# Kernel tuning notes

Hardware: AMD Instinct MI355X
Metric: run time of the kernel (lower is better)

## Reference

```python
import jax, jax.numpy as jnp
import numpy as np

EPS = 1e-5

def mish(x):
    return x * jnp.tanh(jax.nn.softplus(x))

def masked_bn(x, masks, w, b, rm, rv):
    # eval-mode masked batchnorm: normalize with running stats, zero masked-out positions
    out = w * ((x - rm) / jnp.sqrt(rv + EPS)) + b
    return jnp.where(masks, out, jnp.zeros((), dtype=out.dtype))

def channel_shuffle(x):
    B, C, L = x.shape
    cpg = C // 2
    y = jnp.pad(x, ((0, 0), (1, 1), (0, 0)))          # [B, C+2, L]
    y = y.reshape(B, 2, cpg + 1, L)
    y = jnp.transpose(y, (0, 2, 1, 3)).reshape(B, -1, L)
    return y[:, 1:-1, :]

def setup_inputs() -> dict:
    key = jax.random.key(0)
    ks = jax.random.split(key, 8)
    B, C, L = 32, 512, 4096
    br = C // 2
    x = jax.random.normal(ks[0], (B, C, L), dtype=jnp.float32)
    masks = jax.random.randint(ks[1], (B, 1, L), 0, 2) > 0
    s = 1.0 / np.sqrt(br)
    w1 = jax.random.normal(ks[2], (br, br, 1), dtype=jnp.float32) * s
    w2 = jax.random.normal(ks[3], (br, 1, 3), dtype=jnp.float32) * (1.0 / np.sqrt(3.0))
    w3 = jax.random.normal(ks[4], (br, br, 1), dtype=jnp.float32) * s
    def bn_params(k):
        k1, k2 = jax.random.split(k)
        return (jnp.ones((br, 1), jnp.float32), jnp.zeros((br, 1), jnp.float32),
                jax.random.normal(k1, (br, 1), jnp.float32) * 0.1,
                jnp.abs(jax.random.normal(k2, (br, 1), jnp.float32)) * 0.1 + 0.9)
    bn1 = bn_params(ks[5]); bn2 = bn_params(ks[6]); bn3 = bn_params(ks[7])
    return {"x": x, "masks": masks, "w1": w1, "w2": w2, "w3": w3,
            "bn1_w": bn1[0], "bn1_b": bn1[1], "bn1_rm": bn1[2], "bn1_rv": bn1[3],
            "bn2_w": bn2[0], "bn2_b": bn2[1], "bn2_rm": bn2[2], "bn2_rv": bn2[3],
            "bn3_w": bn3[0], "bn3_b": bn3[1], "bn3_rm": bn3[2], "bn3_rv": bn3[3]}

def reference(x, masks, w1, w2, w3,
              bn1_w, bn1_b, bn1_rm, bn1_rv,
              bn2_w, bn2_b, bn2_rm, bn2_rv,
              bn3_w, bn3_b, bn3_rm, bn3_rv):
    C = x.shape[1]
    x1, x2 = x[:, :C // 2, :], x[:, C // 2:, :]
    br = C // 2
    # conv_1: 1x1 pointwise -> GEMM
    b2 = jnp.einsum('oi,bil->bol', w1[:, :, 0], x2)
    b2 = mish(b2)
    b2 = masked_bn(b2, masks, bn1_w, bn1_b, bn1_rm, bn1_rv)
    # conv_2: depthwise k=3, pad=1
    b2 = jax.lax.conv_general_dilated(
        b2, w2, window_strides=(1,), padding=((1, 1),),
        dimension_numbers=('NCH', 'OIH', 'NCH'), feature_group_count=br)
    b2 = masked_bn(b2, masks, bn2_w, bn2_b, bn2_rm, bn2_rv)
    # conv_3: 1x1 pointwise
    b2 = jnp.einsum('oi,bil->bol', w3[:, :, 0], b2)
    b2 = mish(b2)
    b2 = masked_bn(b2, masks, bn3_w, bn3_b, bn3_rm, bn3_rv)
    # dropout: identity in eval mode
    out = jnp.concatenate([x1, b2], axis=1)
    return channel_shuffle(out)
```

## Files before the change

kernel.cpp:

```cpp
#include <hip/hip_runtime.h>
#include <cmath>

#define BATCH 32
#define CIN   512
#define BR    256
#define LEN   4096
#define TL    32
#define ROWS  34
#define RS    264
#define NBLK  128

typedef __attribute__((ext_vector_type(8))) short bf16x8;
typedef __attribute__((ext_vector_type(4))) float f32x4;

#define MFMA_BF16(a,b,c) __builtin_amdgcn_mfma_f32_16x16x32_bf16((a),(b),(c),0,0,0)

__device__ __forceinline__ float bf2f(unsigned short h){
  union { unsigned int u; float f; } c; c.u = ((unsigned int)h) << 16; return c.f;
}
__device__ __forceinline__ unsigned short f2bf(float f){
  union { float f; unsigned int u; } c; c.f = f;
  unsigned int r = c.u + 0x7fffu + ((c.u >> 16) & 1u);
  return (unsigned short)(r >> 16);
}
__device__ __forceinline__ float mish_f(float v){
  float p = __expf(fminf(v, 40.0f));
  float u = p * (p + 2.0f);
  return v * (u / (u + 2.0f));
}
__device__ __forceinline__ void unpack8(const uint4 v, float* f){
  f[0] = bf2f((unsigned short)(v.x & 0xffffu)); f[1] = bf2f((unsigned short)(v.x >> 16));
  f[2] = bf2f((unsigned short)(v.y & 0xffffu)); f[3] = bf2f((unsigned short)(v.y >> 16));
  f[4] = bf2f((unsigned short)(v.z & 0xffffu)); f[5] = bf2f((unsigned short)(v.z >> 16));
  f[6] = bf2f((unsigned short)(v.w & 0xffffu)); f[7] = bf2f((unsigned short)(v.w >> 16));
}

__global__ void prep_kernel(const float* __restrict__ w1, const float* __restrict__ w2,
                            const float* __restrict__ w3,
                            const float* __restrict__ b1w, const float* __restrict__ b1b,
                            const float* __restrict__ b1rm, const float* __restrict__ b1rv,
                            const float* __restrict__ b2w, const float* __restrict__ b2b,
                            const float* __restrict__ b2rm, const float* __restrict__ b2rv,
                            const float* __restrict__ b3w, const float* __restrict__ b3b,
                            const float* __restrict__ b3rm, const float* __restrict__ b3rv,
                            unsigned short* __restrict__ w1bf, unsigned short* __restrict__ w3bf,
                            float* __restrict__ folds)
{
  const int g = blockIdx.x * 256 + threadIdx.x;
  w1bf[g] = f2bf(w1[g]);
  w3bf[g] = f2bf(w3[g]);
  if (blockIdx.x == 0) {
    const int c = threadIdx.x;
    float a1 = b1w[c] / sqrtf(b1rv[c] + 1e-5f);
    folds[c]        = a1; folds[256 + c]  = b1b[c] - b1rm[c] * a1;
    float a2 = b2w[c] / sqrtf(b2rv[c] + 1e-5f);
    folds[512 + c]  = a2; folds[768 + c]  = b2b[c] - b2rm[c] * a2;
    float a3 = b3w[c] / sqrtf(b3rv[c] + 1e-5f);
    folds[1024 + c] = a3; folds[1280 + c] = b3b[c] - b3rm[c] * a3;
    folds[1536 + c] = w2[c * 3 + 0];
    folds[1792 + c] = w2[c * 3 + 1];
    folds[2048 + c] = w2[c * 3 + 2];
  }
}

__global__ __launch_bounds__(256, 4)
void fused_main(const float* __restrict__ xg,
                const int*   __restrict__ maskg,
                const unsigned short* __restrict__ w1bf,
                const unsigned short* __restrict__ w3bf,
                const float* __restrict__ fa1, const float* __restrict__ fb1,
                const float* __restrict__ fa2, const float* __restrict__ fb2,
                const float* __restrict__ fa3, const float* __restrict__ fb3,
                const float* __restrict__ w2p,
                float*       __restrict__ outg)
{
  __shared__ __align__(16) unsigned short ls_x2[ROWS * RS];
  __shared__ __align__(16) unsigned short ls_t1[ROWS * RS];

  const int tid = threadIdx.x;
  const int bx  = blockIdx.x;
  const int b   = blockIdx.y;
  const int l0  = bx * TL;

  {
    const size_t nchunks = (size_t)BATCH * BR * LEN / 4;
    const size_t stride  = (size_t)NBLK * BATCH * 256;
    for (size_t idx = ((size_t)b * NBLK + bx) * 256 + tid; idx < nchunks; idx += stride) {
      const int l  = (int)((idx & 1023) * 4);
      const int c  = (int)((idx >> 10) & 255);
      const int bb = (int)(idx >> 18);
      const float4 v = *(const float4*)(xg + (size_t)(bb * CIN + c) * LEN + l);
      *(float4*)(outg + (size_t)(bb * CIN + 2 * c + 1) * LEN + l) = v;
    }
  }

  if (bx == 0 || bx == NBLK - 1) {
    uint4* z = (uint4*)ls_x2;
    const uint4 zz = make_uint4(0, 0, 0, 0);
    for (int i = tid; i < (ROWS * RS) / 8; i += 256) z[i] = zz;
  }
  __syncthreads();

  {
    const int lbase4 = l0 - 4;
    for (int q = tid; q < 256 * 10; q += 256) {
      const int c   = q / 10;
      const int j   = q - c * 10;
      const int lg  = lbase4 + j * 4;
      const int lgc = min(max(lg, 0), LEN - 4);
      const float4 v = *(const float4*)(xg + (size_t)(b * CIN + BR + c) * LEN + lgc);
      const float vv[4] = {v.x, v.y, v.z, v.w};
      #pragma unroll
      for (int jj = 0; jj < 4; ++jj) {
        const int p = (lgc + jj) - (l0 - 1);
        if (p >= 0 && p < ROWS) ls_x2[p * RS + c] = f2bf(vv[jj]);
      }
    }
  }
  __syncthreads();

  const int lane = tid & 63;
  const int wid  = tid >> 6;
  const int xl   = lane & 15;
  const int qd   = lane >> 4;

  {
    int mk1[3];
    #pragma unroll
    for (int j = 0; j < 3; ++j) {
      const int p = 16 * j + xl;
      const int l = l0 - 1 + p;
      mk1[j] = (p < ROWS && l >= 0 && l < LEN) ? maskg[b * LEN + l] : 0;
    }
    #pragma unroll
    for (int mi = 0; mi < 4; ++mi) {
      const int ob = (wid * 4 + mi) * 16;
      bf16x8 af[8];
      #pragma unroll
      for (int k = 0; k < 8; ++k)
        af[k] = *(const bf16x8*)&w1bf[(size_t)(ob + xl) * 256 + k * 32 + qd * 8];
      const f32x4 av = *(const f32x4*)&fa1[ob + 4 * qd];
      const f32x4 bv = *(const f32x4*)&fb1[ob + 4 * qd];
      #pragma unroll
      for (int j = 0; j < 3; ++j) {
        const int p  = 16 * j + xl;
        const int rp = min(p, ROWS - 1);
        bf16x8 bfr[8];
        #pragma unroll
        for (int k = 0; k < 8; ++k)
          bfr[k] = *(const bf16x8*)&ls_x2[rp * RS + k * 32 + qd * 8];
        f32x4 acc = {0.f, 0.f, 0.f, 0.f};
        #pragma unroll
        for (int k = 0; k < 8; ++k) acc = MFMA_BF16(af[k], bfr[k], acc);
        unsigned short us[4];
        #pragma unroll
        for (int r = 0; r < 4; ++r) {
          float v = mish_f(acc[r]);
          v = av[r] * v + bv[r];
          if (!mk1[j]) v = 0.0f;
          us[r] = f2bf(v);
        }
        if (p < ROWS) {
          const unsigned int lo = (unsigned int)us[0] | ((unsigned int)us[1] << 16);
          const unsigned int hi = (unsigned int)us[2] | ((unsigned int)us[3] << 16);
          *(uint2*)&ls_t1[p * RS + ob + 4 * qd] = make_uint2(lo, hi);
        }
      }
    }
  }
  __syncthreads();

  {
    const int c0    = (tid & 31) * 8;
    const int qbase = tid >> 5;
    const f32x4 k0a = *(const f32x4*)&w2p[      c0], k0b = *(const f32x4*)&w2p[      c0 + 4];
    const f32x4 k1a = *(const f32x4*)&w2p[256 + c0], k1b = *(const f32x4*)&w2p[256 + c0 + 4];
    const f32x4 k2a = *(const f32x4*)&w2p[512 + c0], k2b = *(const f32x4*)&w2p[512 + c0 + 4];
    const f32x4 a2a = *(const f32x4*)&fa2[c0],       a2b = *(const f32x4*)&fa2[c0 + 4];
    const f32x4 b2a = *(const f32x4*)&fb2[c0],       b2b = *(const f32x4*)&fb2[c0 + 4];
    #pragma unroll
    for (int it = 0; it < 4; ++it) {
      const int qo = qbase + 8 * it;
      const int mk = maskg[b * LEN + l0 + qo];
      const uint4 ra = *(const uint4*)&ls_t1[(qo    ) * RS + c0];
      const uint4 rb = *(const uint4*)&ls_t1[(qo + 1) * RS + c0];
      const uint4 rc = *(const uint4*)&ls_t1[(qo + 2) * RS + c0];
      float ta[8], tb[8], tc[8];
      unpack8(ra, ta); unpack8(rb, tb); unpack8(rc, tc);
      unsigned short us[8];
      #pragma unroll
      for (int i = 0; i < 4; ++i) {
        float y  = a2a[i] * (k0a[i] * ta[i]     + k1a[i] * tb[i]     + k2a[i] * tc[i]    ) + b2a[i];
        float y2 = a2b[i] * (k0b[i] * ta[4 + i] + k1b[i] * tb[4 + i] + k2b[i] * tc[4 + i]) + b2b[i];
        if (!mk) { y = 0.0f; y2 = 0.0f; }
        us[i]     = f2bf(y);
        us[4 + i] = f2bf(y2);
      }
      uint4 wv;
      wv.x = (unsigned int)us[0] | ((unsigned int)us[1] << 16);
      wv.y = (unsigned int)us[2] | ((unsigned int)us[3] << 16);
      wv.z = (unsigned int)us[4] | ((unsigned int)us[5] << 16);
      wv.w = (unsigned int)us[6] | ((unsigned int)us[7] << 16);
      *(uint4*)&ls_x2[qo * RS + c0] = wv;
    }
  }
  __syncthreads();

  {
    int4 mku[2];
    #pragma unroll
    for (int j = 0; j < 2; ++j)
      mku[j] = *(const int4*)&maskg[b * LEN + l0 + 16 * j + 4 * qd];
    #pragma unroll
    for (int mi = 0; mi < 4; ++mi) {
      const int ob = (wid * 4 + mi) * 16;
      bf16x8 af[8];
      #pragma unroll
      for (int k = 0; k < 8; ++k)
        af[k] = *(const bf16x8*)&w3bf[(size_t)(ob + xl) * 256 + k * 32 + qd * 8];
      const float a3v = fa3[ob + xl];
      const float b3v = fb3[ob + xl];
      #pragma unroll
      for (int j = 0; j < 2; ++j) {
        bf16x8 ta2[8];
        #pragma unroll
        for (int k = 0; k < 8; ++k)
          ta2[k] = *(const bf16x8*)&ls_x2[(16 * j + xl) * RS + k * 32 + qd * 8];
        f32x4 acc = {0.f, 0.f, 0.f, 0.f};
        #pragma unroll
        for (int k = 0; k < 8; ++k) acc = MFMA_BF16(ta2[k], af[k], acc);
        const int4 mk = mku[j];
        const int mks[4] = {mk.x, mk.y, mk.z, mk.w};
        float4 ov;
        float* op = &ov.x;
        #pragma unroll
        for (int r = 0; r < 4; ++r) {
          float v = mish_f(acc[r]);
          v = a3v * v + b3v;
          if (!mks[r]) v = 0.0f;
          op[r] = v;
        }
        *(float4*)&outg[(size_t)(b * CIN + 2 * (ob + xl)) * LEN + l0 + 16 * j + 4 * qd] = ov;
      }
    }
  }
}

extern "C" void kernel_launch(void* const* d_in, const int* in_sizes, int n_in,
                              void* d_out, int out_size, void* d_ws, size_t ws_size,
                              hipStream_t stream) {
  (void)in_sizes; (void)n_in; (void)out_size; (void)ws_size;
  const float* xg    = (const float*)d_in[0];
  const int*   maskg = (const int*)d_in[1];
  const float* w1    = (const float*)d_in[2];
  const float* w2    = (const float*)d_in[3];
  const float* w3    = (const float*)d_in[4];
  const float* b1w   = (const float*)d_in[5];
  const float* b1b   = (const float*)d_in[6];
  const float* b1rm  = (const float*)d_in[7];
  const float* b1rv  = (const float*)d_in[8];
  const float* b2w   = (const float*)d_in[9];
  const float* b2b   = (const float*)d_in[10];
  const float* b2rm  = (const float*)d_in[11];
  const float* b2rv  = (const float*)d_in[12];
  const float* b3w   = (const float*)d_in[13];
  const float* b3b   = (const float*)d_in[14];
  const float* b3rm  = (const float*)d_in[15];
  const float* b3rv  = (const float*)d_in[16];
  float* outp = (float*)d_out;

  unsigned short* w1bf = (unsigned short*)d_ws;
  unsigned short* w3bf = (unsigned short*)((char*)d_ws + 131072);
  float*          folds = (float*)((char*)d_ws + 262144);

  hipLaunchKernelGGL(prep_kernel, dim3(256), dim3(256), 0, stream,
                     w1, w2, w3,
                     b1w, b1b, b1rm, b1rv, b2w, b2b, b2rm, b2rv, b3w, b3b, b3rm, b3rv,
                     w1bf, w3bf, folds);

  hipLaunchKernelGGL(fused_main, dim3(NBLK, BATCH, 1), dim3(256, 1, 1), 0, stream,
                     xg, maskg, w1bf, w3bf,
                     folds, folds + 256,
                     folds + 512, folds + 768,
                     folds + 1024, folds + 1280,
                     folds + 1536,
                     outp);
}
```

Baseline: 600.5 us.

## Split x1 passthrough copy into separate kernel, prefetch x2 tile, stage masks in LDS

Moves the x1 channel-interleave copy out of the fused kernel into a dedicated streaming copy kernel, so the fused kernel no longer runs a grid-stride copy loop. The x2 tile loads are issued up front into registers before the zero-fill and barrier, so they overlap with that work. Masks are loaded once per block into shared memory and reused by all three stages instead of being re-read from global memory. The cost is one extra kernel launch, and the fused kernel now holds ten float4 values in registers, which raises register pressure at its occupancy target of four blocks per SM.

```diff
diff --git a/kernel.cpp b/kernel.cpp
--- a/kernel.cpp
+++ b/kernel.cpp
@@ -63,6 +63,25 @@
   }
 }
 
+__global__ __launch_bounds__(256)
+void copy_x1_kernel(const float* __restrict__ xg, float* __restrict__ outg)
+{
+  const int k  = blockIdx.x;
+  const int bb = k >> 8;
+  const int c  = k & 255;
+  const float4* __restrict__ src = (const float4*)(xg  + (size_t)(bb * CIN + c)         * LEN);
+  float4*       __restrict__ dst = (float4*)      (outg + (size_t)(bb * CIN + 2 * c + 1) * LEN);
+  const int t = threadIdx.x;
+  const float4 v0 = src[t];
+  const float4 v1 = src[t + 256];
+  const float4 v2 = src[t + 512];
+  const float4 v3 = src[t + 768];
+  dst[t]       = v0;
+  dst[t + 256] = v1;
+  dst[t + 512] = v2;
+  dst[t + 768] = v3;
+}
+
 __global__ __launch_bounds__(256, 4)
 void fused_main(const float* __restrict__ xg,
                 const int*   __restrict__ maskg,
@@ -76,22 +95,22 @@
 {
   __shared__ __align__(16) unsigned short ls_x2[ROWS * RS];
   __shared__ __align__(16) unsigned short ls_t1[ROWS * RS];
+  __shared__ int ls_mk[48];
 
   const int tid = threadIdx.x;
   const int bx  = blockIdx.x;
   const int b   = blockIdx.y;
   const int l0  = bx * TL;
 
-  {
-    const size_t nchunks = (size_t)BATCH * BR * LEN / 4;
-    const size_t stride  = (size_t)NBLK * BATCH * 256;
-    for (size_t idx = ((size_t)b * NBLK + bx) * 256 + tid; idx < nchunks; idx += stride) {
-      const int l  = (int)((idx & 1023) * 4);
-      const int c  = (int)((idx >> 10) & 255);
-      const int bb = (int)(idx >> 18);
-      const float4 v = *(const float4*)(xg + (size_t)(bb * CIN + c) * LEN + l);
-      *(float4*)(outg + (size_t)(bb * CIN + 2 * c + 1) * LEN + l) = v;
-    }
+  float4 stg[10];
+  #pragma unroll
+  for (int it = 0; it < 10; ++it) {
+    const int q   = tid + 256 * it;
+    const int c   = q / 10;
+    const int j   = q - 10 * c;
+    const int lg  = l0 - 4 + 4 * j;
+    const int lgc = min(max(lg, 0), LEN - 4);
+    stg[it] = *(const float4*)(xg + (size_t)(b * CIN + BR + c) * LEN + lgc);
   }
 
   if (bx == 0 || bx == NBLK - 1) {
@@ -99,22 +118,24 @@
     const uint4 zz = make_uint4(0, 0, 0, 0);
     for (int i = tid; i < (ROWS * RS) / 8; i += 256) z[i] = zz;
   }
+  if (tid < 48) {
+    const int l = l0 - 1 + tid;
+    ls_mk[tid] = (tid < ROWS && l >= 0 && l < LEN) ? maskg[b * LEN + l] : 0;
+  }
   __syncthreads();
 
-  {
-    const int lbase4 = l0 - 4;
-    for (int q = tid; q < 256 * 10; q += 256) {
-      const int c   = q / 10;
-      const int j   = q - c * 10;
-      const int lg  = lbase4 + j * 4;
-      const int lgc = min(max(lg, 0), LEN - 4);
-      const float4 v = *(const float4*)(xg + (size_t)(b * CIN + BR + c) * LEN + lgc);
-      const float vv[4] = {v.x, v.y, v.z, v.w};
-      #pragma unroll
-      for (int jj = 0; jj < 4; ++jj) {
-        const int p = (lgc + jj) - (l0 - 1);
-        if (p >= 0 && p < ROWS) ls_x2[p * RS + c] = f2bf(vv[jj]);
-      }
+  #pragma unroll
+  for (int it = 0; it < 10; ++it) {
+    const int q   = tid + 256 * it;
+    const int c   = q / 10;
+    const int j   = q - 10 * c;
+    const int lg  = l0 - 4 + 4 * j;
+    const int lgc = min(max(lg, 0), LEN - 4);
+    const float vv[4] = {stg[it].x, stg[it].y, stg[it].z, stg[it].w};
+    #pragma unroll
+    for (int jj = 0; jj < 4; ++jj) {
+      const int p = (lgc + jj) - (l0 - 1);
+      if (p >= 0 && p < ROWS) ls_x2[p * RS + c] = f2bf(vv[jj]);
     }
   }
   __syncthreads();
@@ -127,11 +148,8 @@
   {
     int mk1[3];
     #pragma unroll
-    for (int j = 0; j < 3; ++j) {
-      const int p = 16 * j + xl;
-      const int l = l0 - 1 + p;
-      mk1[j] = (p < ROWS && l >= 0 && l < LEN) ? maskg[b * LEN + l] : 0;
-    }
+    for (int j = 0; j < 3; ++j)
+      mk1[j] = ls_mk[16 * j + xl];
     #pragma unroll
     for (int mi = 0; mi < 4; ++mi) {
       const int ob = (wid * 4 + mi) * 16;
@@ -181,7 +199,7 @@
     #pragma unroll
     for (int it = 0; it < 4; ++it) {
       const int qo = qbase + 8 * it;
-      const int mk = maskg[b * LEN + l0 + qo];
+      const int mk = ls_mk[1 + qo];
       const uint4 ra = *(const uint4*)&ls_t1[(qo    ) * RS + c0];
       const uint4 rb = *(const uint4*)&ls_t1[(qo + 1) * RS + c0];
       const uint4 rc = *(const uint4*)&ls_t1[(qo + 2) * RS + c0];
@@ -207,10 +225,12 @@
   __syncthreads();
 
   {
-    int4 mku[2];
+    int mks[2][4];
     #pragma unroll
     for (int j = 0; j < 2; ++j)
-      mku[j] = *(const int4*)&maskg[b * LEN + l0 + 16 * j + 4 * qd];
+      #pragma unroll
+      for (int r = 0; r < 4; ++r)
+        mks[j][r] = ls_mk[1 + 16 * j + 4 * qd + r];
     #pragma unroll
     for (int mi = 0; mi < 4; ++mi) {
       const int ob = (wid * 4 + mi) * 16;
@@ -229,15 +249,13 @@
         f32x4 acc = {0.f, 0.f, 0.f, 0.f};
         #pragma unroll
         for (int k = 0; k < 8; ++k) acc = MFMA_BF16(ta2[k], af[k], acc);
-        const int4 mk = mku[j];
-        const int mks[4] = {mk.x, mk.y, mk.z, mk.w};
         float4 ov;
         float* op = &ov.x;
         #pragma unroll
         for (int r = 0; r < 4; ++r) {
           float v = mish_f(acc[r]);
           v = a3v * v + b3v;
-          if (!mks[r]) v = 0.0f;
+          if (!mks[j][r]) v = 0.0f;
           op[r] = v;
         }
         *(float4*)&outg[(size_t)(b * CIN + 2 * (ob + xl)) * LEN + l0 + 16 * j + 4 * qd] = ov;
@@ -278,6 +296,9 @@
                      b1w, b1b, b1rm, b1rv, b2w, b2b, b2rm, b2rv, b3w, b3b, b3rm, b3rv,
                      w1bf, w3bf, folds);
 
+  hipLaunchKernelGGL(copy_x1_kernel, dim3(BATCH * BR), dim3(256, 1, 1), 0, stream,
+                     xg, outp);
+
   hipLaunchKernelGGL(fused_main, dim3(NBLK, BATCH, 1), dim3(256, 1, 1), 0, stream,
                      xg, maskg, w1bf, w3bf,
                      folds, folds + 256,
```

After: 595.9 us. About the same (-0.8%).
